# Optimization experiments

Measured on AMD Instinct MI355X. Metric: run time of the kernel, lower is better.

## Reference

```python
import jax, jax.numpy as jnp
import numpy as np

NUM_ROUTES = 1152
NUM_CAPS = 10
CAPS_IN = 8
CAPS_DIM = 16
BATCH = 128
NUM_IT = 3


def _squash(s):
    # s: [..., caps_dim]; scale = |s|^2 / ((1+|s|^2) * |s|)
    sqn = jnp.sum(s * s, axis=-1, keepdims=True)
    return s * (sqn / ((1.0 + sqn) * jnp.sqrt(sqn)))


def setup_inputs() -> dict:
    key = jax.random.key(0)
    k1, k2 = jax.random.split(key)
    x = jax.random.normal(k1, (BATCH, NUM_ROUTES, CAPS_IN), dtype=jnp.float32)
    W = jax.random.normal(k2, (1, NUM_ROUTES, NUM_CAPS, CAPS_DIM, CAPS_IN), dtype=jnp.float32)
    return {"input": x, "W": W}


def reference(input, W):
    # u_hat[b,r,j,d] = W[r,j,d,c] @ x[b,r,c]  (original broadcasts W over batch)
    u_hat = jnp.einsum('rjdc,brc->brjd', W[0], input)
    r, j = u_hat.shape[1], u_hat.shape[2]
    b_ij = jnp.zeros((r, j), dtype=u_hat.dtype)  # shared across batch, as in original
    v = None
    for _ in range(NUM_IT):
        c_ij = jax.nn.softmax(b_ij, axis=1)          # softmax over num_caps (dim=2 orig)
        s = jnp.einsum('rj,brjd->bjd', c_ij, u_hat)  # weighted sum over routes
        v = _squash(s)                                # [bs, num_caps, caps_dim]
        # agreement: <u_hat, v> averaged over batch (original updates every iter)
        b_ij = b_ij + jnp.mean(jnp.einsum('brjd,bjd->brj', u_hat, v), axis=0)
    return v[..., None]  # [bs, num_caps, caps_dim, 1], matches v_j.squeeze(1) shape
```

## Files before the change

### kernel.cpp

```cpp
#include <hip/hip_runtime.h>
#include <math.h>

#define R_ROUTES 1152
#define N_CAPS 10
#define C_IN 8
#define D_DIM 16
#define B_BATCH 128
#define JD 160
#define KK 9216
#define KSPLIT 48
#define RS 24
#define NG 5
#define BH 2

typedef __attribute__((ext_vector_type(8))) short short8;
typedef __attribute__((ext_vector_type(4))) float f32x4;

__device__ inline unsigned short f2bf(float f) {
    unsigned int u = __float_as_uint(f);
    unsigned int r = u + 0x7FFFu + ((u >> 16) & 1u);
    return (unsigned short)(r >> 16);
}
__device__ inline float bf2f(unsigned short h) {
    return __uint_as_float(((unsigned int)h) << 16);
}


__global__ __launch_bounds__(256) void k_prep(
    const float* __restrict__ x, unsigned short* __restrict__ xh,
    unsigned short* __restrict__ xl, unsigned short* __restrict__ xT,
    float* __restrict__ b_ij, float* __restrict__ s_all) {
    __shared__ float tile[32][33];
    int bx = blockIdx.x;
    int by = blockIdx.y;
    int t = threadIdx.x;
    int tx = t & 31, ty = t >> 5;
#pragma unroll
    for (int i = 0; i < 4; i++) {
        int row = ty + i * 8;
        size_t idx = (size_t)(by * 32 + row) * KK + bx * 32 + tx;
        float v = x[idx];
        tile[row][tx] = v;
        unsigned short hi = f2bf(v);
        xh[idx] = hi;
        xl[idx] = f2bf(v - bf2f(hi));
    }
    __syncthreads();
#pragma unroll
    for (int i = 0; i < 4; i++) {
        int row = ty + i * 8;
        xT[(size_t)(bx * 32 + row) * B_BATCH + by * 32 + tx] = f2bf(tile[tx][row]);
    }
    int bid = by * 288 + bx;
    if (bid < 240) s_all[bid * 256 + t] = 0.f;
    else if (bid < 285) b_ij[(bid - 240) * 256 + t] = 0.f;
}

template <bool FIRST>
__global__ __launch_bounds__(256) void k_iter(
    const unsigned short* __restrict__ xh, const unsigned short* __restrict__ xl,
    const float* __restrict__ W, const float* __restrict__ b_ij,
    float* __restrict__ s) {
    __shared__ float cs[RS][N_CAPS];
    __shared__ unsigned short bhs[32][200];
    int t = threadIdx.x;
    int ks = blockIdx.x, ng = blockIdx.y, bh = blockIdx.z;
    int r0 = ks * RS, jd0 = ng * 32, b_base = bh * 64;

    if (!FIRST && t < RS) {
        float bj[N_CAPS], m = -1e30f;
#pragma unroll
        for (int j = 0; j < N_CAPS; j++) { bj[j] = b_ij[(r0 + t) * N_CAPS + j]; m = fmaxf(m, bj[j]); }
        float sum = 0.f;
#pragma unroll
        for (int j = 0; j < N_CAPS; j++) { bj[j] = expf(bj[j] - m); sum += bj[j]; }
        float inv = 1.f / sum;
#pragma unroll
        for (int j = 0; j < N_CAPS; j++) cs[t][j] = bj[j] * inv;
    }
    __syncthreads();

#pragma unroll
    for (int p = t; p < RS * 32; p += 256) {
        int rl = p >> 5, jdl = p & 31;
        const float* wp = W + ((size_t)(r0 + rl) * JD + jd0 + jdl) * C_IN;
        float c = FIRST ? 0.1f : cs[rl][(jd0 + jdl) >> 4];
        short8 vh;
#pragma unroll
        for (int i = 0; i < 8; i++) vh[i] = (short)f2bf(wp[i] * c);
        *(short8*)&bhs[jdl][rl * 8] = vh;
    }
    __syncthreads();

    int w = t >> 6, l = t & 63, row = l & 15, quad = l >> 4;
    const short8* pah = (const short8*)(xh + (size_t)(b_base + w * 16 + row) * KK + ks * 192);
    const short8* pal = (const short8*)(xl + (size_t)(b_base + w * 16 + row) * KK + ks * 192);
    f32x4 acc0 = {0,0,0,0}, acc1 = {0,0,0,0};
#pragma unroll
    for (int st = 0; st < 6; st++) {
        short8 Bh0 = *(const short8*)&bhs[row][st * 32 + quad * 8];
        short8 Bh1 = *(const short8*)&bhs[16 + row][st * 32 + quad * 8];
        short8 Ah = pah[st * 4 + quad], Al = pal[st * 4 + quad];
        acc0 = __builtin_amdgcn_mfma_f32_16x16x32_bf16(Ah, Bh0, acc0, 0, 0, 0);
        acc0 = __builtin_amdgcn_mfma_f32_16x16x32_bf16(Al, Bh0, acc0, 0, 0, 0);
        acc1 = __builtin_amdgcn_mfma_f32_16x16x32_bf16(Ah, Bh1, acc1, 0, 0, 0);
        acc1 = __builtin_amdgcn_mfma_f32_16x16x32_bf16(Al, Bh1, acc1, 0, 0, 0);
    }
#pragma unroll
    for (int i = 0; i < 4; i++) {
        int b0 = b_base + w * 16 + quad * 4 + i;
        atomicAdd(&s[(size_t)b0 * JD + jd0 + row],      acc0[i]);
        atomicAdd(&s[(size_t)b0 * JD + jd0 + 16 + row], acc1[i]);
    }
}

__global__ __launch_bounds__(256) void k_va(
    const unsigned short* __restrict__ xT, const float* __restrict__ s,
    const float* __restrict__ W, float* __restrict__ b_ij) {
    __shared__ unsigned short vb[JD][136];
    __shared__ float m2[32][164];
    int t = threadIdx.x;
    int r0 = blockIdx.x * 4, rc0 = blockIdx.x * 32;

#pragma unroll
    for (int q = 0; q < 5; q++) {
        int pi = t * 5 + q;
        int b = pi / N_CAPS, j = pi % N_CAPS;
        const float* sp = s + (size_t)b * JD + j * D_DIM;
        float sv[D_DIM], sqn = 0.f;
#pragma unroll
        for (int d = 0; d < D_DIM; d++) { sv[d] = sp[d]; sqn = fmaf(sv[d], sv[d], sqn); }
        float scale = sqn / ((1.f + sqn) * sqrtf(sqn));
#pragma unroll
        for (int d = 0; d < D_DIM; d++)
            vb[j * D_DIM + d][b] = f2bf(sv[d] * scale);
    }
    __syncthreads();

    int w = t >> 6, l = t & 63, row = l & 15, quad = l >> 4;
    for (int u = w; u < 20; u += 4) {
        int mt = u / 10, nt = u % 10;
        const short8* pa = (const short8*)(xT + (size_t)(rc0 + mt * 16 + row) * B_BATCH);
        f32x4 acc = {0,0,0,0};
#pragma unroll
        for (int st = 0; st < 4; st++) {
            short8 Bv = *(const short8*)&vb[nt * 16 + row][st * 32 + quad * 8];
            acc = __builtin_amdgcn_mfma_f32_16x16x32_bf16(pa[st * 4 + quad], Bv, acc, 0, 0, 0);
        }
#pragma unroll
        for (int i = 0; i < 4; i++)
            m2[mt * 16 + quad * 4 + i][nt * 16 + row] = acc[i];
    }
    __syncthreads();

    for (int p = t; p < 640; p += 256) {
        int rl = p / JD, jd = p % JD;
        const float* wp = W + ((size_t)(r0 + rl) * JD + jd) * C_IN;
        float a = 0.f;
#pragma unroll
        for (int c = 0; c < C_IN; c++)
            a = fmaf(wp[c], m2[rl * 8 + c][jd], a);
#pragma unroll
        for (int off = 1; off < 16; off <<= 1) a += __shfl_xor(a, off, 16);
        if ((jd & 15) == 0)
            b_ij[(r0 + rl) * N_CAPS + (jd >> 4)] += a * (1.f / B_BATCH);
    }
}

__global__ __launch_bounds__(320) void k_rs_final(
    const float* __restrict__ s, float* __restrict__ out) {
    int t = threadIdx.x;
    int bloc = t / JD, jd = t % JD;
    int b = blockIdx.x * 2 + bloc;
    float acc = s[(size_t)b * JD + jd];
    float sq = acc * acc;
#pragma unroll
    for (int off = 1; off < 16; off <<= 1) sq += __shfl_xor(sq, off, 16);
    float scale = sq / ((1.f + sq) * sqrtf(sq));
    out[(size_t)b * JD + jd] = acc * scale;
}

extern "C" void kernel_launch(void* const* d_in, const int* in_sizes, int n_in,
                              void* d_out, int out_size, void* d_ws, size_t ws_size,
                              hipStream_t stream) {
    const float* x = (const float*)d_in[0];
    const float* W = (const float*)d_in[1];
    float* out = (float*)d_out;
    char* ws = (char*)d_ws;

    float*          b_ij = (float*)(ws + 0);
    float*          s0   = (float*)(ws + 46080);
    float*          s1   = (float*)(ws + 46080 + 81920);
    float*          s2   = (float*)(ws + 46080 + 163840);
    unsigned short* xh   = (unsigned short*)(ws + 292096);
    unsigned short* xl   = (unsigned short*)(ws + 2651392);
    unsigned short* xT   = (unsigned short*)(ws + 5010688);

    k_prep<<<dim3(288, 4), 256, 0, stream>>>(x, xh, xl, xT, b_ij, s0);

    k_iter<true><<<dim3(KSPLIT, NG, BH), 256, 0, stream>>>(xh, xl, W, b_ij, s0);
    k_va<<<288, 256, 0, stream>>>(xT, s0, W, b_ij);

    k_iter<false><<<dim3(KSPLIT, NG, BH), 256, 0, stream>>>(xh, xl, W, b_ij, s1);
    k_va<<<288, 256, 0, stream>>>(xT, s1, W, b_ij);

    k_iter<false><<<dim3(KSPLIT, NG, BH), 256, 0, stream>>>(xh, xl, W, b_ij, s2);
    k_rs_final<<<64, 320, 0, stream>>>(s2, out);
}
```

Before: 111.9 us.

## Fuse agreement update, softmax and routing GEMM into one kernel per iteration

Merges the agreement/b_ij update kernel into the next routing-sum kernel. Each block recomputes the squash of the previous s and the agreement for only its own 24 routes, then computes the softmax locally and builds the scaled W tile. The final squash runs in the last-arriving block, tracked by an atomic counter, which removes the separate final kernel. This cuts the launch count from 7 to 4. In exchange, each block redundantly squashes all 128x10 capsules and recomputes the agreement across all ng/bh blocks, which duplicates work 10x.

```diff
diff --git a/kernel.cpp b/kernel.cpp
--- a/kernel.cpp
+++ b/kernel.cpp
@@ -12,6 +12,7 @@
 #define RS 24
 #define NG 5
 #define BH 2
+#define NBLK (KSPLIT * NG * BH)
 
 typedef __attribute__((ext_vector_type(8))) short short8;
 typedef __attribute__((ext_vector_type(4))) float f32x4;
@@ -29,7 +30,8 @@
 __global__ __launch_bounds__(256) void k_prep(
     const float* __restrict__ x, unsigned short* __restrict__ xh,
     unsigned short* __restrict__ xl, unsigned short* __restrict__ xT,
-    float* __restrict__ b_ij, float* __restrict__ s_all) {
+    float* __restrict__ b_ij, float* __restrict__ s_all,
+    unsigned int* __restrict__ cnt) {
     __shared__ float tile[32][33];
     int bx = blockIdx.x;
     int by = blockIdx.y;
@@ -54,40 +56,24 @@
     int bid = by * 288 + bx;
     if (bid < 240) s_all[bid * 256 + t] = 0.f;
     else if (bid < 285) b_ij[(bid - 240) * 256 + t] = 0.f;
-}
-
-template <bool FIRST>
-__global__ __launch_bounds__(256) void k_iter(
+    else if (bid == 285 && t == 0) *cnt = 0u;
+}
+
+__global__ __launch_bounds__(256) void k_iter1(
     const unsigned short* __restrict__ xh, const unsigned short* __restrict__ xl,
-    const float* __restrict__ W, const float* __restrict__ b_ij,
-    float* __restrict__ s) {
-    __shared__ float cs[RS][N_CAPS];
+    const float* __restrict__ W, float* __restrict__ s) {
     __shared__ unsigned short bhs[32][200];
     int t = threadIdx.x;
     int ks = blockIdx.x, ng = blockIdx.y, bh = blockIdx.z;
     int r0 = ks * RS, jd0 = ng * 32, b_base = bh * 64;
 
-    if (!FIRST && t < RS) {
-        float bj[N_CAPS], m = -1e30f;
-#pragma unroll
-        for (int j = 0; j < N_CAPS; j++) { bj[j] = b_ij[(r0 + t) * N_CAPS + j]; m = fmaxf(m, bj[j]); }
-        float sum = 0.f;
-#pragma unroll
-        for (int j = 0; j < N_CAPS; j++) { bj[j] = expf(bj[j] - m); sum += bj[j]; }
-        float inv = 1.f / sum;
-#pragma unroll
-        for (int j = 0; j < N_CAPS; j++) cs[t][j] = bj[j] * inv;
-    }
-    __syncthreads();
-
 #pragma unroll
     for (int p = t; p < RS * 32; p += 256) {
         int rl = p >> 5, jdl = p & 31;
         const float* wp = W + ((size_t)(r0 + rl) * JD + jd0 + jdl) * C_IN;
-        float c = FIRST ? 0.1f : cs[rl][(jd0 + jdl) >> 4];
         short8 vh;
 #pragma unroll
-        for (int i = 0; i < 8; i++) vh[i] = (short)f2bf(wp[i] * c);
+        for (int i = 0; i < 8; i++) vh[i] = (short)f2bf(wp[i] * 0.1f);
         *(short8*)&bhs[jdl][rl * 8] = vh;
     }
     __syncthreads();
@@ -114,19 +100,28 @@
     }
 }
 
-__global__ __launch_bounds__(256) void k_va(
-    const unsigned short* __restrict__ xT, const float* __restrict__ s,
-    const float* __restrict__ W, float* __restrict__ b_ij) {
+template <int WRITE_B, int LAST>
+__global__ __launch_bounds__(256) void k_fused(
+    const unsigned short* __restrict__ xh, const unsigned short* __restrict__ xl,
+    const unsigned short* __restrict__ xT, const float* __restrict__ W,
+    float* __restrict__ b_ij, const float* __restrict__ s_prev,
+    float* __restrict__ s_cur, unsigned int* __restrict__ cnt,
+    float* __restrict__ out) {
     __shared__ unsigned short vb[JD][136];
-    __shared__ float m2[32][164];
+    __shared__ unsigned short bhs[32][200];
+    __shared__ float bupd[RS][N_CAPS];
+    __shared__ float cs[RS][N_CAPS];
+    __shared__ unsigned int lastflag;
+
     int t = threadIdx.x;
-    int r0 = blockIdx.x * 4, rc0 = blockIdx.x * 32;
+    int ks = blockIdx.x, ng = blockIdx.y, bh = blockIdx.z;
+    int r0 = ks * RS, jd0 = ng * 32, b_base = bh * 64;
 
 #pragma unroll
     for (int q = 0; q < 5; q++) {
         int pi = t * 5 + q;
         int b = pi / N_CAPS, j = pi % N_CAPS;
-        const float* sp = s + (size_t)b * JD + j * D_DIM;
+        const float* sp = s_prev + (size_t)b * JD + j * D_DIM;
         float sv[D_DIM], sqn = 0.f;
 #pragma unroll
         for (int d = 0; d < D_DIM; d++) { sv[d] = sp[d]; sqn = fmaf(sv[d], sv[d], sqn); }
@@ -138,46 +133,110 @@
     __syncthreads();
 
     int w = t >> 6, l = t & 63, row = l & 15, quad = l >> 4;
-    for (int u = w; u < 20; u += 4) {
-        int mt = u / 10, nt = u % 10;
+    int rhalf = l >> 5, cbase = (quad & 1) * 4;
+
+    int rc0 = ks * 192;
+    for (int mt = 0; mt < 12; mt++) {
         const short8* pa = (const short8*)(xT + (size_t)(rc0 + mt * 16 + row) * B_BATCH);
-        f32x4 acc = {0,0,0,0};
-#pragma unroll
-        for (int st = 0; st < 4; st++) {
-            short8 Bv = *(const short8*)&vb[nt * 16 + row][st * 32 + quad * 8];
-            acc = __builtin_amdgcn_mfma_f32_16x16x32_bf16(pa[st * 4 + quad], Bv, acc, 0, 0, 0);
-        }
-#pragma unroll
-        for (int i = 0; i < 4; i++)
-            m2[mt * 16 + quad * 4 + i][nt * 16 + row] = acc[i];
-    }
-    __syncthreads();
-
-    for (int p = t; p < 640; p += 256) {
-        int rl = p / JD, jd = p % JD;
-        const float* wp = W + ((size_t)(r0 + rl) * JD + jd) * C_IN;
-        float a = 0.f;
-#pragma unroll
-        for (int c = 0; c < C_IN; c++)
-            a = fmaf(wp[c], m2[rl * 8 + c][jd], a);
-#pragma unroll
-        for (int off = 1; off < 16; off <<= 1) a += __shfl_xor(a, off, 16);
-        if ((jd & 15) == 0)
-            b_ij[(r0 + rl) * N_CAPS + (jd >> 4)] += a * (1.f / B_BATCH);
-    }
-}
-
-__global__ __launch_bounds__(320) void k_rs_final(
-    const float* __restrict__ s, float* __restrict__ out) {
-    int t = threadIdx.x;
-    int bloc = t / JD, jd = t % JD;
-    int b = blockIdx.x * 2 + bloc;
-    float acc = s[(size_t)b * JD + jd];
-    float sq = acc * acc;
-#pragma unroll
-    for (int off = 1; off < 16; off <<= 1) sq += __shfl_xor(sq, off, 16);
-    float scale = sq / ((1.f + sq) * sqrtf(sq));
-    out[(size_t)b * JD + jd] = acc * scale;
+        short8 af0 = pa[quad], af1 = pa[4 + quad], af2 = pa[8 + quad], af3 = pa[12 + quad];
+        for (int nt = (w + mt) & 3; nt < N_CAPS; nt += 4) {
+            f32x4 acc = {0,0,0,0};
+            acc = __builtin_amdgcn_mfma_f32_16x16x32_bf16(af0, *(const short8*)&vb[nt * 16 + row][quad * 8], acc, 0, 0, 0);
+            acc = __builtin_amdgcn_mfma_f32_16x16x32_bf16(af1, *(const short8*)&vb[nt * 16 + row][32 + quad * 8], acc, 0, 0, 0);
+            acc = __builtin_amdgcn_mfma_f32_16x16x32_bf16(af2, *(const short8*)&vb[nt * 16 + row][64 + quad * 8], acc, 0, 0, 0);
+            acc = __builtin_amdgcn_mfma_f32_16x16x32_bf16(af3, *(const short8*)&vb[nt * 16 + row][96 + quad * 8], acc, 0, 0, 0);
+            const float* wp = W + ((size_t)(r0 + 2 * mt + rhalf) * JD + nt * 16 + row) * C_IN + cbase;
+            float4 w4 = *(const float4*)wp;
+            float part = acc[0] * w4.x + acc[1] * w4.y + acc[2] * w4.z + acc[3] * w4.w;
+#pragma unroll
+            for (int off = 1; off < 32; off <<= 1) part += __shfl_xor(part, off, 32);
+            if ((l & 31) == 0) bupd[2 * mt + rhalf][nt] = part * (1.f / (float)B_BATCH);
+        }
+    }
+    __syncthreads();
+
+    if (t < RS) {
+        float braw[N_CAPS];
+        float m = -1e30f;
+#pragma unroll
+        for (int j = 0; j < N_CAPS; j++) {
+            float base = WRITE_B ? 0.f : b_ij[(r0 + t) * N_CAPS + j];
+            braw[j] = base + bupd[t][j];
+            m = fmaxf(m, braw[j]);
+        }
+        float e[N_CAPS], sum = 0.f;
+#pragma unroll
+        for (int j = 0; j < N_CAPS; j++) { e[j] = expf(braw[j] - m); sum += e[j]; }
+        float inv = 1.f / sum;
+#pragma unroll
+        for (int j = 0; j < N_CAPS; j++) cs[t][j] = e[j] * inv;
+        if (WRITE_B && ng == 0 && bh == 0) {
+#pragma unroll
+            for (int j = 0; j < N_CAPS; j++) b_ij[(r0 + t) * N_CAPS + j] = braw[j];
+        }
+    }
+    __syncthreads();
+
+#pragma unroll
+    for (int p = t; p < RS * 32; p += 256) {
+        int rl = p >> 5, jdl = p & 31;
+        const float* wp = W + ((size_t)(r0 + rl) * JD + jd0 + jdl) * C_IN;
+        float c = cs[rl][(jd0 + jdl) >> 4];
+        short8 vh;
+#pragma unroll
+        for (int i = 0; i < 8; i++) vh[i] = (short)f2bf(wp[i] * c);
+        *(short8*)&bhs[jdl][rl * 8] = vh;
+    }
+    __syncthreads();
+
+    const short8* pah = (const short8*)(xh + (size_t)(b_base + w * 16 + row) * KK + ks * 192);
+    const short8* pal = (const short8*)(xl + (size_t)(b_base + w * 16 + row) * KK + ks * 192);
+    f32x4 acc0 = {0,0,0,0}, acc1 = {0,0,0,0};
+#pragma unroll
+    for (int st = 0; st < 6; st++) {
+        short8 Bh0 = *(const short8*)&bhs[row][st * 32 + quad * 8];
+        short8 Bh1 = *(const short8*)&bhs[16 + row][st * 32 + quad * 8];
+        short8 Ah = pah[st * 4 + quad], Al = pal[st * 4 + quad];
+        acc0 = __builtin_amdgcn_mfma_f32_16x16x32_bf16(Ah, Bh0, acc0, 0, 0, 0);
+        acc0 = __builtin_amdgcn_mfma_f32_16x16x32_bf16(Al, Bh0, acc0, 0, 0, 0);
+        acc1 = __builtin_amdgcn_mfma_f32_16x16x32_bf16(Ah, Bh1, acc1, 0, 0, 0);
+        acc1 = __builtin_amdgcn_mfma_f32_16x16x32_bf16(Al, Bh1, acc1, 0, 0, 0);
+    }
+#pragma unroll
+    for (int i = 0; i < 4; i++) {
+        int b0 = b_base + w * 16 + quad * 4 + i;
+        atomicAdd(&s_cur[(size_t)b0 * JD + jd0 + row],      acc0[i]);
+        atomicAdd(&s_cur[(size_t)b0 * JD + jd0 + 16 + row], acc1[i]);
+    }
+
+    if (LAST) {
+        __syncthreads();
+        if (t == 0) {
+            __threadfence();
+            unsigned int old = atomicAdd(cnt, 1u);
+            lastflag = (old == (unsigned)(NBLK - 1)) ? 1u : 0u;
+        }
+        __syncthreads();
+        if (lastflag) {
+            __threadfence();
+#pragma unroll
+            for (int q = 0; q < 5; q++) {
+                int pi = t * 5 + q;
+                int b = pi / N_CAPS, j = pi % N_CAPS;
+                float* sp = s_cur + (size_t)b * JD + j * D_DIM;
+                float sv[D_DIM], sqn = 0.f;
+#pragma unroll
+                for (int d = 0; d < D_DIM; d++) {
+                    sv[d] = __hip_atomic_load(sp + d, __ATOMIC_RELAXED, __HIP_MEMORY_SCOPE_AGENT);
+                    sqn = fmaf(sv[d], sv[d], sqn);
+                }
+                float scale = sqn / ((1.f + sqn) * sqrtf(sqn));
+#pragma unroll
+                for (int d = 0; d < D_DIM; d++)
+                    out[(size_t)b * JD + j * D_DIM + d] = sv[d] * scale;
+            }
+        }
+    }
 }
 
 extern "C" void kernel_launch(void* const* d_in, const int* in_sizes, int n_in,
@@ -192,18 +251,18 @@
     float*          s0   = (float*)(ws + 46080);
     float*          s1   = (float*)(ws + 46080 + 81920);
     float*          s2   = (float*)(ws + 46080 + 163840);
+    unsigned int*   cnt  = (unsigned int*)(ws + 291840);
     unsigned short* xh   = (unsigned short*)(ws + 292096);
     unsigned short* xl   = (unsigned short*)(ws + 2651392);
     unsigned short* xT   = (unsigned short*)(ws + 5010688);
 
-    k_prep<<<dim3(288, 4), 256, 0, stream>>>(x, xh, xl, xT, b_ij, s0);
-
-    k_iter<true><<<dim3(KSPLIT, NG, BH), 256, 0, stream>>>(xh, xl, W, b_ij, s0);
-    k_va<<<288, 256, 0, stream>>>(xT, s0, W, b_ij);
-
-    k_iter<false><<<dim3(KSPLIT, NG, BH), 256, 0, stream>>>(xh, xl, W, b_ij, s1);
-    k_va<<<288, 256, 0, stream>>>(xT, s1, W, b_ij);
-
-    k_iter<false><<<dim3(KSPLIT, NG, BH), 256, 0, stream>>>(xh, xl, W, b_ij, s2);
-    k_rs_final<<<64, 320, 0, stream>>>(s2, out);
-}
+    k_prep<<<dim3(288, 4), 256, 0, stream>>>(x, xh, xl, xT, b_ij, s0, cnt);
+
+    k_iter1<<<dim3(KSPLIT, NG, BH), 256, 0, stream>>>(xh, xl, W, s0);
+
+    k_fused<1, 0><<<dim3(KSPLIT, NG, BH), 256, 0, stream>>>(
+        xh, xl, xT, W, b_ij, s0, s1, cnt, out);
+
+    k_fused<0, 1><<<dim3(KSPLIT, NG, BH), 256, 0, stream>>>(
+        xh, xl, xT, W, b_ij, s1, s2, cnt, out);
+}
```

Result: slower. 150.4 us (+34.4%).

## Fuse squash into last-block epilogue of routing kernel, drop final kernel

Applied to the files above, without the earlier changes.

Each routing-iteration kernel now counts finished blocks with an atomic counter, and the last block to finish computes the squash of the accumulated s. It writes v as a bf16 transposed matrix, or writes the final output directly on the last iteration. This removes the separate final squash kernel. It also removes the per-block recomputation of squash in the agreement kernel, which now reads the precomputed vT from global memory. The cost is one serial tail block per iteration, plus reuse of the output buffer as scratch for vT.

```diff
diff --git a/kernel.cpp b/kernel.cpp
--- a/kernel.cpp
+++ b/kernel.cpp
@@ -12,6 +12,7 @@
 #define RS 24
 #define NG 5
 #define BH 2
+#define NBLK (KSPLIT * NG * BH)
 
 typedef __attribute__((ext_vector_type(8))) short short8;
 typedef __attribute__((ext_vector_type(4))) float f32x4;
@@ -29,7 +30,8 @@
 __global__ __launch_bounds__(256) void k_prep(
     const float* __restrict__ x, unsigned short* __restrict__ xh,
     unsigned short* __restrict__ xl, unsigned short* __restrict__ xT,
-    float* __restrict__ b_ij, float* __restrict__ s_all) {
+    float* __restrict__ b_ij, float* __restrict__ s_all,
+    unsigned int* __restrict__ cnt) {
     __shared__ float tile[32][33];
     int bx = blockIdx.x;
     int by = blockIdx.y;
@@ -54,15 +56,18 @@
     int bid = by * 288 + bx;
     if (bid < 240) s_all[bid * 256 + t] = 0.f;
     else if (bid < 285) b_ij[(bid - 240) * 256 + t] = 0.f;
-}
-
-template <bool FIRST>
+    else if (bid == 285 && t < 3) cnt[t] = 0u;
+}
+
+template <int FIRST, int SQ>
 __global__ __launch_bounds__(256) void k_iter(
     const unsigned short* __restrict__ xh, const unsigned short* __restrict__ xl,
     const float* __restrict__ W, const float* __restrict__ b_ij,
-    float* __restrict__ s) {
+    float* __restrict__ s, unsigned int* __restrict__ cnt,
+    unsigned short* __restrict__ vT, float* __restrict__ out) {
     __shared__ float cs[RS][N_CAPS];
     __shared__ unsigned short bhs[32][200];
+    __shared__ unsigned int lastflag;
     int t = threadIdx.x;
     int ks = blockIdx.x, ng = blockIdx.y, bh = blockIdx.z;
     int r0 = ks * RS, jd0 = ng * 32, b_base = bh * 64;
@@ -112,41 +117,57 @@
         atomicAdd(&s[(size_t)b0 * JD + jd0 + row],      acc0[i]);
         atomicAdd(&s[(size_t)b0 * JD + jd0 + 16 + row], acc1[i]);
     }
-}
-
-__global__ __launch_bounds__(256) void k_va(
-    const unsigned short* __restrict__ xT, const float* __restrict__ s,
+
+    __syncthreads();
+    if (t == 0) {
+        __threadfence();
+        unsigned int old = atomicAdd(cnt, 1u);
+        lastflag = (old == (unsigned)(NBLK - 1)) ? 1u : 0u;
+    }
+    __syncthreads();
+    if (lastflag) {
+        __threadfence();
+#pragma unroll
+        for (int q = 0; q < 5; q++) {
+            int pi = t * 5 + q;
+            int b = pi / N_CAPS, j = pi % N_CAPS;
+            float* sp = s + (size_t)b * JD + j * D_DIM;
+            float sv[D_DIM], sqn = 0.f;
+#pragma unroll
+            for (int d = 0; d < D_DIM; d++) {
+                sv[d] = __hip_atomic_load(sp + d, __ATOMIC_RELAXED, __HIP_MEMORY_SCOPE_AGENT);
+                sqn = fmaf(sv[d], sv[d], sqn);
+            }
+            float scale = sqn / ((1.f + sqn) * sqrtf(sqn));
+            if (SQ == 1) {
+#pragma unroll
+                for (int d = 0; d < D_DIM; d++)
+                    vT[(size_t)(j * D_DIM + d) * B_BATCH + b] = f2bf(sv[d] * scale);
+            } else {
+#pragma unroll
+                for (int d = 0; d < D_DIM; d++)
+                    out[(size_t)b * JD + j * D_DIM + d] = sv[d] * scale;
+            }
+        }
+    }
+}
+
+__global__ __launch_bounds__(256) void k_ag(
+    const unsigned short* __restrict__ xT, const unsigned short* __restrict__ vT,
     const float* __restrict__ W, float* __restrict__ b_ij) {
-    __shared__ unsigned short vb[JD][136];
     __shared__ float m2[32][164];
     int t = threadIdx.x;
     int r0 = blockIdx.x * 4, rc0 = blockIdx.x * 32;
-
-#pragma unroll
-    for (int q = 0; q < 5; q++) {
-        int pi = t * 5 + q;
-        int b = pi / N_CAPS, j = pi % N_CAPS;
-        const float* sp = s + (size_t)b * JD + j * D_DIM;
-        float sv[D_DIM], sqn = 0.f;
-#pragma unroll
-        for (int d = 0; d < D_DIM; d++) { sv[d] = sp[d]; sqn = fmaf(sv[d], sv[d], sqn); }
-        float scale = sqn / ((1.f + sqn) * sqrtf(sqn));
-#pragma unroll
-        for (int d = 0; d < D_DIM; d++)
-            vb[j * D_DIM + d][b] = f2bf(sv[d] * scale);
-    }
-    __syncthreads();
 
     int w = t >> 6, l = t & 63, row = l & 15, quad = l >> 4;
     for (int u = w; u < 20; u += 4) {
         int mt = u / 10, nt = u % 10;
         const short8* pa = (const short8*)(xT + (size_t)(rc0 + mt * 16 + row) * B_BATCH);
+        const short8* pb = (const short8*)(vT + (size_t)(nt * D_DIM + row) * B_BATCH);
         f32x4 acc = {0,0,0,0};
 #pragma unroll
-        for (int st = 0; st < 4; st++) {
-            short8 Bv = *(const short8*)&vb[nt * 16 + row][st * 32 + quad * 8];
-            acc = __builtin_amdgcn_mfma_f32_16x16x32_bf16(pa[st * 4 + quad], Bv, acc, 0, 0, 0);
-        }
+        for (int st = 0; st < 4; st++)
+            acc = __builtin_amdgcn_mfma_f32_16x16x32_bf16(pa[st * 4 + quad], pb[st * 4 + quad], acc, 0, 0, 0);
 #pragma unroll
         for (int i = 0; i < 4; i++)
             m2[mt * 16 + quad * 4 + i][nt * 16 + row] = acc[i];
@@ -165,19 +186,6 @@
         if ((jd & 15) == 0)
             b_ij[(r0 + rl) * N_CAPS + (jd >> 4)] += a * (1.f / B_BATCH);
     }
-}
-
-__global__ __launch_bounds__(320) void k_rs_final(
-    const float* __restrict__ s, float* __restrict__ out) {
-    int t = threadIdx.x;
-    int bloc = t / JD, jd = t % JD;
-    int b = blockIdx.x * 2 + bloc;
-    float acc = s[(size_t)b * JD + jd];
-    float sq = acc * acc;
-#pragma unroll
-    for (int off = 1; off < 16; off <<= 1) sq += __shfl_xor(sq, off, 16);
-    float scale = sq / ((1.f + sq) * sqrtf(sq));
-    out[(size_t)b * JD + jd] = acc * scale;
 }
 
 extern "C" void kernel_launch(void* const* d_in, const int* in_sizes, int n_in,
@@ -192,18 +200,22 @@
     float*          s0   = (float*)(ws + 46080);
     float*          s1   = (float*)(ws + 46080 + 81920);
     float*          s2   = (float*)(ws + 46080 + 163840);
+    unsigned int*   cnt  = (unsigned int*)(ws + 291840);
     unsigned short* xh   = (unsigned short*)(ws + 292096);
     unsigned short* xl   = (unsigned short*)(ws + 2651392);
     unsigned short* xT   = (unsigned short*)(ws + 5010688);
-
-    k_prep<<<dim3(288, 4), 256, 0, stream>>>(x, xh, xl, xT, b_ij, s0);
-
-    k_iter<true><<<dim3(KSPLIT, NG, BH), 256, 0, stream>>>(xh, xl, W, b_ij, s0);
-    k_va<<<288, 256, 0, stream>>>(xT, s0, W, b_ij);
-
-    k_iter<false><<<dim3(KSPLIT, NG, BH), 256, 0, stream>>>(xh, xl, W, b_ij, s1);
-    k_va<<<288, 256, 0, stream>>>(xT, s1, W, b_ij);
-
-    k_iter<false><<<dim3(KSPLIT, NG, BH), 256, 0, stream>>>(xh, xl, W, b_ij, s2);
-    k_rs_final<<<64, 320, 0, stream>>>(s2, out);
-}
+    unsigned short* vT   = (unsigned short*)d_out;
+
+    k_prep<<<dim3(288, 4), 256, 0, stream>>>(x, xh, xl, xT, b_ij, s0, cnt);
+
+    k_iter<1, 1><<<dim3(KSPLIT, NG, BH), 256, 0, stream>>>(
+        xh, xl, W, b_ij, s0, cnt + 0, vT, out);
+    k_ag<<<288, 256, 0, stream>>>(xT, vT, W, b_ij);
+
+    k_iter<0, 1><<<dim3(KSPLIT, NG, BH), 256, 0, stream>>>(
+        xh, xl, W, b_ij, s1, cnt + 1, vT, out);
+    k_ag<<<288, 256, 0, stream>>>(xT, vT, W, b_ij);
+
+    k_iter<0, 2><<<dim3(KSPLIT, NG, BH), 256, 0, stream>>>(
+        xh, xl, W, b_ij, s2, cnt + 2, vT, out);
+}
```

Result: slower. 176.8 us (+57.9%).
